# Kernel tuning notes

Measured on AMD Instinct MI355X. Metric: run time of the kernel, lower is better.

The kernel has to match this reference:

```python
import jax, jax.numpy as jnp
import numpy as np

EPS_GIN = 0.0      # GINConv eps (train_eps=False)
EPS_LN = 1e-5      # LayerNorm eps
EPS_GN = 1e-5      # GraphNorm eps


def _layer_norm(h, w, b):
    mu = jnp.mean(h, axis=-1, keepdims=True)
    var = jnp.mean(jnp.square(h - mu), axis=-1, keepdims=True)
    return (h - mu) * jax.lax.rsqrt(var + EPS_LN) * w + b


def setup_inputs() -> dict:
    key = jax.random.key(0)
    ks = jax.random.split(key, 6)
    N, E, C = 50000, 800000, 64
    x = jax.random.normal(ks[0], (N, C), dtype=jnp.float32)
    edge_index = jax.random.randint(ks[1], (2, E), 0, N, dtype=jnp.int64)
    W0 = jax.random.normal(ks[2], (C, C), dtype=jnp.float32) / np.sqrt(C)
    W1 = jax.random.normal(ks[3], (C, C), dtype=jnp.float32) / np.sqrt(C)
    ln0_w = jnp.ones((C,), jnp.float32); ln0_b = jnp.zeros((C,), jnp.float32)
    ln1_w = jnp.ones((C,), jnp.float32); ln1_b = jnp.zeros((C,), jnp.float32)
    # GraphNorm params
    gn_w = jnp.ones((C,), jnp.float32)
    gn_b = jnp.zeros((C,), jnp.float32)
    gn_alpha = jnp.ones((C,), jnp.float32)  # mean_scale
    return {"x": x, "edge_index": edge_index, "W0": W0, "ln0_w": ln0_w,
            "ln0_b": ln0_b, "W1": W1, "ln1_w": ln1_w, "ln1_b": ln1_b,
            "gn_w": gn_w, "gn_b": gn_b, "gn_alpha": gn_alpha}


def reference(x, edge_index, W0, ln0_w, ln0_b, W1, ln1_w, ln1_b, gn_w, gn_b, gn_alpha):
    N = x.shape[0]
    src, dst = edge_index[0], edge_index[1]
    # GINConv aggregation: sum of source-node features at each target node
    agg = jax.ops.segment_sum(x[src], dst, num_segments=N)  # [N, C]
    h = (1.0 + EPS_GIN) * x + agg
    # MLP: (Linear no-bias -> LayerNorm -> ReLU) x 2
    h = jax.nn.relu(_layer_norm(h @ W0.T, ln0_w, ln0_b))
    h = jax.nn.relu(_layer_norm(h @ W1.T, ln1_w, ln1_b))
    # GraphNorm over the single graph (all nodes)
    mean = jnp.mean(h, axis=0, keepdims=True)                # [1, C]
    out = h - gn_alpha * mean
    var = jnp.mean(jnp.square(out), axis=0, keepdims=True)   # [1, C]
    return gn_w * out * jax.lax.rsqrt(var + EPS_GN) + gn_b
```

## Files before the change

kernel.cpp:

```cpp
#include <hip/hip_runtime.h>
#include <hip/hip_fp16.h>
#include <stdint.h>

#define LN_EPS 1e-5f
#define GN_EPS 1e-5f

#define NSB 32
#define SLAB1 36864
#define BE1 2048
#define CH2 18
#define NPB2 32
#define SLAB2 768
#define NFB 2048
#define CAP2 768
#define NSLOT 16

__global__ __launch_bounds__(512) void k_sort1_half(
    const uint32_t* __restrict__ ew, int E, int PB1,
    const float* __restrict__ x, uint4* __restrict__ xh8, int n8,
    int* cursors1, uint32_t* pairs1) {
  __shared__ int whist[8 * NSB];
  __shared__ int wbase[8 * NSB];
  __shared__ int wlcur[8 * NSB];
  __shared__ int binStart[NSB], baseG[NSB];
  __shared__ uint32_t stage[BE1];
  const int t = threadIdx.x;

  if (blockIdx.x >= PB1) {
    int i = (blockIdx.x - PB1) * 512 + t;
    if (i >= n8) return;
    float4 a = *(const float4*)&x[i * 8];
    float4 b = *(const float4*)&x[i * 8 + 4];
    __half2 h0 = __floats2half2_rn(a.x, a.y);
    __half2 h1 = __floats2half2_rn(a.z, a.w);
    __half2 h2 = __floats2half2_rn(b.x, b.y);
    __half2 h3 = __floats2half2_rn(b.z, b.w);
    uint4 o;
    o.x = *(uint32_t*)&h0; o.y = *(uint32_t*)&h1;
    o.z = *(uint32_t*)&h2; o.w = *(uint32_t*)&h3;
    xh8[i] = o;
    return;
  }

  const int w = t >> 6;
  const int e0 = blockIdx.x * BE1;
  const int cnt = min(BE1, E - e0);

  uint32_t v = 0;
  if (t < cnt) v = ew[2 * (e0 + t) + 1];
  const int is32 = __syncthreads_or((int)(v != 0));

  if (t < 8 * NSB) { whist[t] = 0; wlcur[t] = 0; }
  __syncthreads();

  uint32_t myP[4];
  #pragma unroll
  for (int r = 0; r < 4; ++r) {
    int i = t + 512 * r;
    if (i < cnt) {
      long long e = e0 + i;
      int s, d;
      if (is32) {
        s = ((const int*)ew)[e];
        d = ((const int*)ew)[(long long)E + e];
      } else {
        s = (int)((const long long*)ew)[e];
        d = (int)((const long long*)ew)[(long long)E + e];
      }
      myP[r] = ((uint32_t)s << 16) | (uint32_t)d;
      atomicAdd(&whist[w * NSB + (d >> 11)], 1);
    }
  }
  __syncthreads();

  if (t < NSB) {
    int sum = 0;
    #pragma unroll
    for (int w2 = 0; w2 < 8; ++w2) {
      wbase[w2 * NSB + t] = sum;
      sum += whist[w2 * NSB + t];
    }
    int s = sum;
    #pragma unroll
    for (int d = 1; d < NSB; d <<= 1) {
      int o = __shfl_up(s, d, NSB);
      if (t >= d) s += o;
    }
    binStart[t] = s - sum;
    baseG[t] = (sum > 0) ? atomicAdd(&cursors1[t], sum) : 0;
  }
  __syncthreads();

  #pragma unroll
  for (int r = 0; r < 4; ++r) {
    int i = t + 512 * r;
    if (i < cnt) {
      int b = (int)(myP[r] & 0xFFFFu) >> 11;
      int p = binStart[b] + wbase[w * NSB + b] +
              atomicAdd(&wlcur[w * NSB + b], 1);
      stage[p] = myP[r];
    }
  }
  __syncthreads();

  for (int i = t; i < cnt; i += 512) {
    uint32_t pr = stage[i];
    int sb = (int)(pr & 0xFFFFu) >> 11;
    int o = baseG[sb] + (i - binStart[sb]);
    if (o < SLAB1) pairs1[(size_t)sb * SLAB1 + o] = pr;
  }
}

__global__ __launch_bounds__(512) void k_part2(const uint32_t* __restrict__ pairs1,
                                               const int* __restrict__ cursors1,
                                               int* cursors2, uint32_t* pairs2) {
  __shared__ int whist[8 * 64];
  __shared__ int wbase[8 * 64];
  __shared__ int wlcur[8 * 64];
  __shared__ int binStart[64], baseG[64];
  __shared__ uint32_t stage[BE1];
  const int t = threadIdx.x;
  const int w = t >> 6;
  const int sb = blockIdx.x / CH2;
  const int ch = blockIdx.x % CH2;
  const int cntS = min(cursors1[sb], SLAB1);
  const int lo = ch * BE1;
  const int cnt = max(0, min(BE1, cntS - lo));
  const uint32_t* src = pairs1 + (size_t)sb * SLAB1 + lo;

  whist[t] = 0;
  wlcur[t] = 0;
  __syncthreads();

  uint32_t my[4];
  #pragma unroll
  for (int r = 0; r < 4; ++r) {
    int i = t + 512 * r;
    if (i < cnt) {
      my[r] = src[i];
      atomicAdd(&whist[(w << 6) + ((my[r] >> 5) & 63)], 1);
    }
  }
  __syncthreads();

  if (t < 64) {
    int sum = 0;
    #pragma unroll
    for (int w2 = 0; w2 < 8; ++w2) {
      wbase[(w2 << 6) + t] = sum;
      sum += whist[(w2 << 6) + t];
    }
    int s = sum;
    #pragma unroll
    for (int d = 1; d < 64; d <<= 1) {
      int o = __shfl_up(s, d, 64);
      if (t >= d) s += o;
    }
    binStart[t] = s - sum;
    baseG[t] = (sum > 0) ? atomicAdd(&cursors2[(sb << 6) + t], sum) : 0;
  }
  __syncthreads();

  #pragma unroll
  for (int r = 0; r < 4; ++r) {
    int i = t + 512 * r;
    if (i < cnt) {
      int b = (int)(my[r] >> 5) & 63;
      int p = binStart[b] + wbase[(w << 6) + b] +
              atomicAdd(&wlcur[(w << 6) + b], 1);
      stage[p] = my[r];
    }
  }
  __syncthreads();

  for (int i = t; i < cnt; i += 512) {
    uint32_t pr = stage[i];
    int sub = (int)(pr >> 5) & 63;
    int o = baseG[sub] + (i - binStart[sub]);
    if (o < SLAB2) pairs2[(size_t)((sb << 6) + sub) * SLAB2 + o] = pr;
  }
}

__global__ __launch_bounds__(256, 8) void k_fused(
    const float4* __restrict__ x4, const uint4* __restrict__ xh8,
    const uint32_t* __restrict__ pairs, const int* __restrict__ cursors,
    const float* __restrict__ W0g, const float* __restrict__ ln0w,
    const float* __restrict__ ln0b, const float* __restrict__ W1g,
    const float* __restrict__ ln1w, const float* __restrict__ ln1b,
    float* __restrict__ out, int N, float* __restrict__ accum) {
  __shared__ __align__(16) float HYt[64 * 33];
  __shared__ __align__(16) float U[2048];
  int* hist = (int*)U;
  int* offs = hist + 32;
  int* lcur = offs + 32;
  int* list = lcur + 32;
  float* Wt = U;
  float* wsum = U;

  const int t = threadIdx.x;
  const int B = blockIdx.x;
  const int cnt = min(cursors[B], SLAB2);
  const uint32_t* pb = pairs + (size_t)B * SLAB2;
  const int node0 = B * NPB2;

  if (t < 32) hist[t] = 0;
  __syncthreads();

  for (int i = t; i < cnt; i += 256) atomicAdd(&hist[pb[i] & 31], 1);
  __syncthreads();

  if (t < 32) {
    int v = hist[t], s = v;
    #pragma unroll
    for (int d = 1; d < 32; d <<= 1) {
      int o = __shfl_up(s, d, 32);
      if (t >= d) s += o;
    }
    offs[t] = s - v;
    lcur[t] = s - v;
  }
  __syncthreads();

  for (int i = t; i < cnt; i += 256) {
    uint32_t p = pb[i];
    int pos = atomicAdd(&lcur[p & 31], 1);
    if (pos < CAP2) list[pos] = (int)(p >> 16);
  }
  __syncthreads();

  const int q8 = t & 7;
  const int nl = t >> 3;
  const int node = node0 + nl;
  float acc[8] = {};
  if (node < N) {
    float4 sa = x4[node * 16 + 2 * q8];
    float4 sb = x4[node * 16 + 2 * q8 + 1];
    acc[0] = sa.x; acc[1] = sa.y; acc[2] = sa.z; acc[3] = sa.w;
    acc[4] = sb.x; acc[5] = sb.y; acc[6] = sb.z; acc[7] = sb.w;
    int j = offs[nl];
    const int e = min(lcur[nl], CAP2);
    for (; j + 3 < e; j += 4) {
      uint4 v0 = xh8[list[j] * 8 + q8];
      uint4 v1 = xh8[list[j + 1] * 8 + q8];
      uint4 v2 = xh8[list[j + 2] * 8 + q8];
      uint4 v3 = xh8[list[j + 3] * 8 + q8];
      #pragma unroll
      for (int c = 0; c < 4; ++c) {
        uint32_t u0 = (&v0.x)[c], u1 = (&v1.x)[c];
        uint32_t u2 = (&v2.x)[c], u3 = (&v3.x)[c];
        float2 f0 = __half22float2(*(__half2*)&u0);
        float2 f1 = __half22float2(*(__half2*)&u1);
        float2 f2 = __half22float2(*(__half2*)&u2);
        float2 f3 = __half22float2(*(__half2*)&u3);
        acc[2 * c]     += (f0.x + f1.x) + (f2.x + f3.x);
        acc[2 * c + 1] += (f0.y + f1.y) + (f2.y + f3.y);
      }
    }
    for (; j < e; ++j) {
      uint4 v0 = xh8[list[j] * 8 + q8];
      #pragma unroll
      for (int c = 0; c < 4; ++c) {
        uint32_t u0 = (&v0.x)[c];
        float2 f0 = __half22float2(*(__half2*)&u0);
        acc[2 * c] += f0.x;
        acc[2 * c + 1] += f0.y;
      }
    }
  }
  __syncthreads();

  #pragma unroll
  for (int c = 0; c < 8; ++c) HYt[(8 * q8 + c) * 33 + nl] = acc[c];

  const int tx = t & 15;
  const int ty = t >> 4;
  const int wc = t & 63, ww = t >> 6;
  float a0[2][4] = {};

  #pragma unroll
  for (int half = 0; half < 2; ++half) {
    {
      #pragma unroll
      for (int r = 0; r < 2; ++r) {
        int k4 = ww * 4 + 16 * r;
        float4 v = *(const float4*)&W0g[wc * 64 + 32 * half + k4];
        Wt[(k4 + 0) * 64 + wc] = v.x; Wt[(k4 + 1) * 64 + wc] = v.y;
        Wt[(k4 + 2) * 64 + wc] = v.z; Wt[(k4 + 3) * 64 + wc] = v.w;
      }
    }
    __syncthreads();
    #pragma unroll 8
    for (int k = 0; k < 32; ++k) {
      float h0 = HYt[(32 * half + k) * 33 + 2 * ty];
      float h1 = HYt[(32 * half + k) * 33 + 2 * ty + 1];
      float4 wv = *(const float4*)&Wt[k * 64 + 4 * tx];
      a0[0][0] += h0 * wv.x; a0[0][1] += h0 * wv.y;
      a0[0][2] += h0 * wv.z; a0[0][3] += h0 * wv.w;
      a0[1][0] += h1 * wv.x; a0[1][1] += h1 * wv.y;
      a0[1][2] += h1 * wv.z; a0[1][3] += h1 * wv.w;
    }
    __syncthreads();
  }

  {
    const float4 lw = *(const float4*)&ln0w[4 * tx];
    const float4 lb = *(const float4*)&ln0b[4 * tx];
    float y[2][4];
    #pragma unroll
    for (int j = 0; j < 2; ++j) {
      float s = a0[j][0] + a0[j][1] + a0[j][2] + a0[j][3];
      #pragma unroll
      for (int m = 1; m < 16; m <<= 1) s += __shfl_xor(s, m, 16);
      float mu = s * (1.f / 64.f);
      float d0 = a0[j][0] - mu, d1 = a0[j][1] - mu;
      float d2 = a0[j][2] - mu, d3 = a0[j][3] - mu;
      float vv = d0 * d0 + d1 * d1 + d2 * d2 + d3 * d3;
      #pragma unroll
      for (int m = 1; m < 16; m <<= 1) vv += __shfl_xor(vv, m, 16);
      float rs = rsqrtf(vv * (1.f / 64.f) + LN_EPS);
      y[j][0] = fmaxf(d0 * rs * lw.x + lb.x, 0.f);
      y[j][1] = fmaxf(d1 * rs * lw.y + lb.y, 0.f);
      y[j][2] = fmaxf(d2 * rs * lw.z + lb.z, 0.f);
      y[j][3] = fmaxf(d3 * rs * lw.w + lb.w, 0.f);
    }
    #pragma unroll
    for (int j = 0; j < 2; ++j) {
      int n = 2 * ty + j;
      HYt[(4 * tx + 0) * 33 + n] = y[j][0];
      HYt[(4 * tx + 1) * 33 + n] = y[j][1];
      HYt[(4 * tx + 2) * 33 + n] = y[j][2];
      HYt[(4 * tx + 3) * 33 + n] = y[j][3];
    }
  }
  __syncthreads();

  float a1[2][4] = {};
  #pragma unroll
  for (int half = 0; half < 2; ++half) {
    {
      #pragma unroll
      for (int r = 0; r < 2; ++r) {
        int k4 = ww * 4 + 16 * r;
        float4 v = *(const float4*)&W1g[wc * 64 + 32 * half + k4];
        Wt[(k4 + 0) * 64 + wc] = v.x; Wt[(k4 + 1) * 64 + wc] = v.y;
        Wt[(k4 + 2) * 64 + wc] = v.z; Wt[(k4 + 3) * 64 + wc] = v.w;
      }
    }
    __syncthreads();
    #pragma unroll 8
    for (int k = 0; k < 32; ++k) {
      float h0 = HYt[(32 * half + k) * 33 + 2 * ty];
      float h1 = HYt[(32 * half + k) * 33 + 2 * ty + 1];
      float4 wv = *(const float4*)&Wt[k * 64 + 4 * tx];
      a1[0][0] += h0 * wv.x; a1[0][1] += h0 * wv.y;
      a1[0][2] += h0 * wv.z; a1[0][3] += h0 * wv.w;
      a1[1][0] += h1 * wv.x; a1[1][1] += h1 * wv.y;
      a1[1][2] += h1 * wv.z; a1[1][3] += h1 * wv.w;
    }
    __syncthreads();
  }

  const float4 lw = *(const float4*)&ln1w[4 * tx];
  const float4 lb = *(const float4*)&ln1b[4 * tx];
  float st1[4] = {0.f, 0.f, 0.f, 0.f}, st2[4] = {0.f, 0.f, 0.f, 0.f};
  #pragma unroll
  for (int j = 0; j < 2; ++j) {
    int nodej = node0 + 2 * ty + j;
    float s = a1[j][0] + a1[j][1] + a1[j][2] + a1[j][3];
    #pragma unroll
    for (int m = 1; m < 16; m <<= 1) s += __shfl_xor(s, m, 16);
    float mu = s * (1.f / 64.f);
    float d0 = a1[j][0] - mu, d1 = a1[j][1] - mu;
    float d2 = a1[j][2] - mu, d3 = a1[j][3] - mu;
    float vv = d0 * d0 + d1 * d1 + d2 * d2 + d3 * d3;
    #pragma unroll
    for (int m = 1; m < 16; m <<= 1) vv += __shfl_xor(vv, m, 16);
    float rs = rsqrtf(vv * (1.f / 64.f) + LN_EPS);
    float y0 = fmaxf(d0 * rs * lw.x + lb.x, 0.f);
    float y1 = fmaxf(d1 * rs * lw.y + lb.y, 0.f);
    float y2 = fmaxf(d2 * rs * lw.z + lb.z, 0.f);
    float y3 = fmaxf(d3 * rs * lw.w + lb.w, 0.f);
    if (nodej < N) {
      *(float4*)&out[(long long)nodej * 64 + 4 * tx] =
          make_float4(y0, y1, y2, y3);
      st1[0] += y0; st2[0] += y0 * y0;
      st1[1] += y1; st2[1] += y1 * y1;
      st1[2] += y2; st2[2] += y2 * y2;
      st1[3] += y3; st2[3] += y3 * y3;
    }
  }
  #pragma unroll
  for (int i = 0; i < 4; ++i) {
    st1[i] += __shfl_xor(st1[i], 16, 64); st1[i] += __shfl_xor(st1[i], 32, 64);
    st2[i] += __shfl_xor(st2[i], 16, 64); st2[i] += __shfl_xor(st2[i], 32, 64);
  }
  const int lane = t & 63, w = t >> 6;
  if (lane < 16) {
    #pragma unroll
    for (int i = 0; i < 4; ++i) {
      wsum[w * 128 + 4 * lane + i] = st1[i];
      wsum[w * 128 + 64 + 4 * lane + i] = st2[i];
    }
  }
  __syncthreads();
  if (t < 128) {
    float s = wsum[t] + wsum[128 + t] + wsum[256 + t] + wsum[384 + t];
    atomicAdd(&accum[(B & (NSLOT - 1)) * 128 + t], s);
  }
}

__global__ __launch_bounds__(256) void k_apply(
    const float4* __restrict__ h4, const float* __restrict__ accum,
    const float* __restrict__ alpha, const float* __restrict__ gnw,
    const float* __restrict__ gnb, float4* __restrict__ outp, int N) {
  __shared__ float cs[128];
  __shared__ float ab[128];
  const int t = threadIdx.x;
  if (t < 128) {
    float s = 0.f;
    #pragma unroll
    for (int sl = 0; sl < NSLOT; ++sl) s += accum[sl * 128 + t];
    cs[t] = s;
  }
  __syncthreads();
  if (t < 64) {
    float invN = 1.f / (float)N;
    float mu = cs[t] * invN;
    float e2 = cs[64 + t] * invN;
    float al = alpha[t];
    float var = e2 - 2.f * al * mu * mu + al * al * mu * mu;
    float a = gnw[t] * rsqrtf(var + GN_EPS);
    ab[t] = a;
    ab[64 + t] = gnb[t] - a * al * mu;
  }
  __syncthreads();
  int idx = blockIdx.x * 256 + t;
  if (idx < N * 16) {
    int q = idx & 15;
    float4 a = *(const float4*)&ab[q * 4];
    float4 b = *(const float4*)&ab[64 + q * 4];
    float4 h = h4[idx];
    outp[idx] = make_float4(a.x * h.x + b.x, a.y * h.y + b.y, a.z * h.z + b.z,
                            a.w * h.w + b.w);
  }
}

extern "C" void kernel_launch(void* const* d_in, const int* in_sizes, int n_in,
                              void* d_out, int out_size, void* d_ws,
                              size_t ws_size, hipStream_t stream) {
  const float* x    = (const float*)d_in[0];
  const void* edges = d_in[1];
  const float* W0   = (const float*)d_in[2];
  const float* ln0w = (const float*)d_in[3];
  const float* ln0b = (const float*)d_in[4];
  const float* W1   = (const float*)d_in[5];
  const float* ln1w = (const float*)d_in[6];
  const float* ln1b = (const float*)d_in[7];
  const float* gnw  = (const float*)d_in[8];
  const float* gnb  = (const float*)d_in[9];
  const float* gna  = (const float*)d_in[10];
  const int N = in_sizes[0] / 64;
  const int E = in_sizes[1] / 2;
  const int nsbU = (N + 2047) >> 11;
  const int nfbU = nsbU << 6;
  const int PB1 = (E + BE1 - 1) / BE1;
  const int HB  = (N * 8 + 511) / 512;

  float* h         = (float*)d_ws;
  uint32_t* pairs1 = (uint32_t*)d_ws;
  uint32_t* pairs2 = (uint32_t*)(h + (size_t)N * 64);
  uint4* xh8       = (uint4*)(pairs2 + (size_t)NFB * SLAB2);
  int* cursors1    = (int*)(xh8 + (size_t)N * 8);
  int* cursors2    = cursors1 + NSB;
  float* accum     = (float*)(cursors2 + NFB);

  hipMemsetAsync(cursors1, 0, (size_t)(NSB + NFB + NSLOT * 128) * 4, stream);
  k_sort1_half<<<PB1 + HB, 512, 0, stream>>>((const uint32_t*)edges, E, PB1,
                                             x, xh8, N * 8, cursors1, pairs1);
  k_part2<<<nsbU * CH2, 512, 0, stream>>>(pairs1, cursors1, cursors2, pairs2);
  k_fused<<<nfbU, 256, 0, stream>>>((const float4*)x, xh8, pairs2, cursors2,
                                    W0, ln0w, ln0b, W1, ln1w, ln1b, h, N,
                                    accum);
  k_apply<<<(N * 16 + 255) / 256, 256, 0, stream>>>((const float4*)h, accum,
                                                    gna, gnw, gnb,
                                                    (float4*)d_out, N);
}
```

Measured before the change: 142.0 us.

## Replace two-pass global edge partition with per-block buckets scanned in fused kernel

Drops the second partition kernel and the global atomic cursors. Each sort block now writes its edges into fixed-capacity per-(block, 1024-node bin) buckets and records the counts, and each fused block scans all source blocks' buckets for its bin, filtering by sub-bin and building per-node lists in LDS. This removes a kernel launch, a memset and a full pass over the pairs, but each fused block reads 32x more pair data than it keeps. The fixed caps of 88 per bucket and 48 per node can silently drop edges under skew. The HYt pitch also changes to 34 so the matmul loop can read float2 values.

```diff
diff --git a/kernel.cpp b/kernel.cpp
--- a/kernel.cpp
+++ b/kernel.cpp
@@ -5,28 +5,29 @@
 #define LN_EPS 1e-5f
 #define GN_EPS 1e-5f
 
-#define NSB 32
-#define SLAB1 36864
+#define NSB 64
 #define BE1 2048
-#define CH2 18
+#define CAP1R 88
 #define NPB2 32
-#define SLAB2 768
-#define NFB 2048
-#define CAP2 768
+#define CAPN 48
 #define NSLOT 16
 
 __global__ __launch_bounds__(512) void k_sort1_half(
     const uint32_t* __restrict__ ew, int E, int PB1,
     const float* __restrict__ x, uint4* __restrict__ xh8, int n8,
-    int* cursors1, uint32_t* pairs1) {
+    float* __restrict__ accum, int* __restrict__ counts1,
+    uint32_t* __restrict__ pairs1) {
   __shared__ int whist[8 * NSB];
   __shared__ int wbase[8 * NSB];
   __shared__ int wlcur[8 * NSB];
-  __shared__ int binStart[NSB], baseG[NSB];
+  __shared__ int binStart[NSB];
   __shared__ uint32_t stage[BE1];
   const int t = threadIdx.x;
 
   if (blockIdx.x >= PB1) {
+    if (blockIdx.x == PB1) {
+      for (int i = t; i < NSLOT * 128; i += 512) accum[i] = 0.f;
+    }
     int i = (blockIdx.x - PB1) * 512 + t;
     if (i >= n8) return;
     float4 a = *(const float4*)&x[i * 8];
@@ -42,15 +43,17 @@
     return;
   }
 
+  const int b = blockIdx.x;
   const int w = t >> 6;
-  const int e0 = blockIdx.x * BE1;
+  const int e0 = b * BE1;
   const int cnt = min(BE1, E - e0);
 
   uint32_t v = 0;
   if (t < cnt) v = ew[2 * (e0 + t) + 1];
   const int is32 = __syncthreads_or((int)(v != 0));
 
-  if (t < 8 * NSB) { whist[t] = 0; wlcur[t] = 0; }
+  whist[t] = 0;
+  wlcur[t] = 0;
   __syncthreads();
 
   uint32_t myP[4];
@@ -68,7 +71,7 @@
         d = (int)((const long long*)ew)[(long long)E + e];
       }
       myP[r] = ((uint32_t)s << 16) | (uint32_t)d;
-      atomicAdd(&whist[w * NSB + (d >> 11)], 1);
+      atomicAdd(&whist[w * NSB + (d >> 10)], 1);
     }
   }
   __syncthreads();
@@ -83,11 +86,11 @@
     int s = sum;
     #pragma unroll
     for (int d = 1; d < NSB; d <<= 1) {
-      int o = __shfl_up(s, d, NSB);
+      int o = __shfl_up(s, d, 64);
       if (t >= d) s += o;
     }
     binStart[t] = s - sum;
-    baseG[t] = (sum > 0) ? atomicAdd(&cursors1[t], sum) : 0;
+    counts1[t * PB1 + b] = sum;
   }
   __syncthreads();
 
@@ -95,9 +98,9 @@
   for (int r = 0; r < 4; ++r) {
     int i = t + 512 * r;
     if (i < cnt) {
-      int b = (int)(myP[r] & 0xFFFFu) >> 11;
-      int p = binStart[b] + wbase[w * NSB + b] +
-              atomicAdd(&wlcur[w * NSB + b], 1);
+      int b2 = (int)(myP[r] & 0xFFFFu) >> 10;
+      int p = binStart[b2] + wbase[w * NSB + b2] +
+              atomicAdd(&wlcur[w * NSB + b2], 1);
       stage[p] = myP[r];
     }
   }
@@ -105,126 +108,51 @@
 
   for (int i = t; i < cnt; i += 512) {
     uint32_t pr = stage[i];
-    int sb = (int)(pr & 0xFFFFu) >> 11;
-    int o = baseG[sb] + (i - binStart[sb]);
-    if (o < SLAB1) pairs1[(size_t)sb * SLAB1 + o] = pr;
-  }
-}
-
-__global__ __launch_bounds__(512) void k_part2(const uint32_t* __restrict__ pairs1,
-                                               const int* __restrict__ cursors1,
-                                               int* cursors2, uint32_t* pairs2) {
-  __shared__ int whist[8 * 64];
-  __shared__ int wbase[8 * 64];
-  __shared__ int wlcur[8 * 64];
-  __shared__ int binStart[64], baseG[64];
-  __shared__ uint32_t stage[BE1];
-  const int t = threadIdx.x;
-  const int w = t >> 6;
-  const int sb = blockIdx.x / CH2;
-  const int ch = blockIdx.x % CH2;
-  const int cntS = min(cursors1[sb], SLAB1);
-  const int lo = ch * BE1;
-  const int cnt = max(0, min(BE1, cntS - lo));
-  const uint32_t* src = pairs1 + (size_t)sb * SLAB1 + lo;
-
-  whist[t] = 0;
-  wlcur[t] = 0;
-  __syncthreads();
-
-  uint32_t my[4];
-  #pragma unroll
-  for (int r = 0; r < 4; ++r) {
-    int i = t + 512 * r;
-    if (i < cnt) {
-      my[r] = src[i];
-      atomicAdd(&whist[(w << 6) + ((my[r] >> 5) & 63)], 1);
-    }
-  }
-  __syncthreads();
-
-  if (t < 64) {
-    int sum = 0;
-    #pragma unroll
-    for (int w2 = 0; w2 < 8; ++w2) {
-      wbase[(w2 << 6) + t] = sum;
-      sum += whist[(w2 << 6) + t];
-    }
-    int s = sum;
-    #pragma unroll
-    for (int d = 1; d < 64; d <<= 1) {
-      int o = __shfl_up(s, d, 64);
-      if (t >= d) s += o;
-    }
-    binStart[t] = s - sum;
-    baseG[t] = (sum > 0) ? atomicAdd(&cursors2[(sb << 6) + t], sum) : 0;
-  }
-  __syncthreads();
-
-  #pragma unroll
-  for (int r = 0; r < 4; ++r) {
-    int i = t + 512 * r;
-    if (i < cnt) {
-      int b = (int)(my[r] >> 5) & 63;
-      int p = binStart[b] + wbase[(w << 6) + b] +
-              atomicAdd(&wlcur[(w << 6) + b], 1);
-      stage[p] = my[r];
-    }
-  }
-  __syncthreads();
-
-  for (int i = t; i < cnt; i += 512) {
-    uint32_t pr = stage[i];
-    int sub = (int)(pr >> 5) & 63;
-    int o = baseG[sub] + (i - binStart[sub]);
-    if (o < SLAB2) pairs2[(size_t)((sb << 6) + sub) * SLAB2 + o] = pr;
+    int sb = (int)(pr & 0xFFFFu) >> 10;
+    int rel = i - binStart[sb];
+    if (rel < CAP1R) pairs1[((size_t)b * NSB + sb) * CAP1R + rel] = pr;
   }
 }
 
 __global__ __launch_bounds__(256, 8) void k_fused(
     const float4* __restrict__ x4, const uint4* __restrict__ xh8,
-    const uint32_t* __restrict__ pairs, const int* __restrict__ cursors,
-    const float* __restrict__ W0g, const float* __restrict__ ln0w,
+    const uint32_t* __restrict__ pairs1, const int* __restrict__ counts1,
+    int PB1, const float* __restrict__ W0g, const float* __restrict__ ln0w,
     const float* __restrict__ ln0b, const float* __restrict__ W1g,
     const float* __restrict__ ln1w, const float* __restrict__ ln1b,
     float* __restrict__ out, int N, float* __restrict__ accum) {
-  __shared__ __align__(16) float HYt[64 * 33];
+  __shared__ __align__(16) float HYt[64 * 34];
   __shared__ __align__(16) float U[2048];
-  int* hist = (int*)U;
-  int* offs = hist + 32;
-  int* lcur = offs + 32;
-  int* list = lcur + 32;
+  int* list32 = (int*)U;
+  int* cnt32 = (int*)U + 32 * CAPN;
+  int* cLDS = (int*)U + 32 * CAPN + 32;
   float* Wt = U;
   float* wsum = U;
 
   const int t = threadIdx.x;
   const int B = blockIdx.x;
-  const int cnt = min(cursors[B], SLAB2);
-  const uint32_t* pb = pairs + (size_t)B * SLAB2;
+  const int sb = B >> 5;
+  const int sub = B & 31;
   const int node0 = B * NPB2;
 
-  if (t < 32) hist[t] = 0;
-  __syncthreads();
-
-  for (int i = t; i < cnt; i += 256) atomicAdd(&hist[pb[i] & 31], 1);
-  __syncthreads();
-
-  if (t < 32) {
-    int v = hist[t], s = v;
-    #pragma unroll
-    for (int d = 1; d < 32; d <<= 1) {
-      int o = __shfl_up(s, d, 32);
-      if (t >= d) s += o;
-    }
-    offs[t] = s - v;
-    lcur[t] = s - v;
-  }
-  __syncthreads();
-
-  for (int i = t; i < cnt; i += 256) {
-    uint32_t p = pb[i];
-    int pos = atomicAdd(&lcur[p & 31], 1);
-    if (pos < CAP2) list[pos] = (int)(p >> 16);
+  if (t < 32) cnt32[t] = 0;
+  for (int i = t; i < PB1; i += 256) cLDS[i] = counts1[sb * PB1 + i];
+  __syncthreads();
+
+  {
+    const int ln64 = t & 63, w4 = t >> 6;
+    for (int blk = w4; blk < PB1; blk += 4) {
+      int c = cLDS[blk];
+      const uint32_t* rp = pairs1 + ((size_t)blk * NSB + sb) * CAP1R;
+      for (int i = ln64; i < c; i += 64) {
+        uint32_t pr = rp[i];
+        if ((int)((pr >> 5) & 31) == sub) {
+          int nloc = (int)(pr & 31);
+          int pos = atomicAdd(&cnt32[nloc], 1);
+          if (pos < CAPN) list32[nloc * CAPN + pos] = (int)(pr >> 16);
+        }
+      }
+    }
   }
   __syncthreads();
 
@@ -234,16 +162,17 @@
   float acc[8] = {};
   if (node < N) {
     float4 sa = x4[node * 16 + 2 * q8];
-    float4 sb = x4[node * 16 + 2 * q8 + 1];
+    float4 sb2 = x4[node * 16 + 2 * q8 + 1];
     acc[0] = sa.x; acc[1] = sa.y; acc[2] = sa.z; acc[3] = sa.w;
-    acc[4] = sb.x; acc[5] = sb.y; acc[6] = sb.z; acc[7] = sb.w;
-    int j = offs[nl];
-    const int e = min(lcur[nl], CAP2);
+    acc[4] = sb2.x; acc[5] = sb2.y; acc[6] = sb2.z; acc[7] = sb2.w;
+    const int e = min(cnt32[nl], CAPN);
+    const int* lp = list32 + nl * CAPN;
+    int j = 0;
     for (; j + 3 < e; j += 4) {
-      uint4 v0 = xh8[list[j] * 8 + q8];
-      uint4 v1 = xh8[list[j + 1] * 8 + q8];
-      uint4 v2 = xh8[list[j + 2] * 8 + q8];
-      uint4 v3 = xh8[list[j + 3] * 8 + q8];
+      uint4 v0 = xh8[lp[j] * 8 + q8];
+      uint4 v1 = xh8[lp[j + 1] * 8 + q8];
+      uint4 v2 = xh8[lp[j + 2] * 8 + q8];
+      uint4 v3 = xh8[lp[j + 3] * 8 + q8];
       #pragma unroll
       for (int c = 0; c < 4; ++c) {
         uint32_t u0 = (&v0.x)[c], u1 = (&v1.x)[c];
@@ -257,7 +186,7 @@
       }
     }
     for (; j < e; ++j) {
-      uint4 v0 = xh8[list[j] * 8 + q8];
+      uint4 v0 = xh8[lp[j] * 8 + q8];
       #pragma unroll
       for (int c = 0; c < 4; ++c) {
         uint32_t u0 = (&v0.x)[c];
@@ -270,7 +199,7 @@
   __syncthreads();
 
   #pragma unroll
-  for (int c = 0; c < 8; ++c) HYt[(8 * q8 + c) * 33 + nl] = acc[c];
+  for (int c = 0; c < 8; ++c) HYt[(8 * q8 + c) * 34 + nl] = acc[c];
 
   const int tx = t & 15;
   const int ty = t >> 4;
@@ -291,13 +220,12 @@
     __syncthreads();
     #pragma unroll 8
     for (int k = 0; k < 32; ++k) {
-      float h0 = HYt[(32 * half + k) * 33 + 2 * ty];
-      float h1 = HYt[(32 * half + k) * 33 + 2 * ty + 1];
+      float2 hh = *(const float2*)&HYt[(32 * half + k) * 34 + 2 * ty];
       float4 wv = *(const float4*)&Wt[k * 64 + 4 * tx];
-      a0[0][0] += h0 * wv.x; a0[0][1] += h0 * wv.y;
-      a0[0][2] += h0 * wv.z; a0[0][3] += h0 * wv.w;
-      a0[1][0] += h1 * wv.x; a0[1][1] += h1 * wv.y;
-      a0[1][2] += h1 * wv.z; a0[1][3] += h1 * wv.w;
+      a0[0][0] += hh.x * wv.x; a0[0][1] += hh.x * wv.y;
+      a0[0][2] += hh.x * wv.z; a0[0][3] += hh.x * wv.w;
+      a0[1][0] += hh.y * wv.x; a0[1][1] += hh.y * wv.y;
+      a0[1][2] += hh.y * wv.z; a0[1][3] += hh.y * wv.w;
     }
     __syncthreads();
   }
@@ -326,10 +254,10 @@
     #pragma unroll
     for (int j = 0; j < 2; ++j) {
       int n = 2 * ty + j;
-      HYt[(4 * tx + 0) * 33 + n] = y[j][0];
-      HYt[(4 * tx + 1) * 33 + n] = y[j][1];
-      HYt[(4 * tx + 2) * 33 + n] = y[j][2];
-      HYt[(4 * tx + 3) * 33 + n] = y[j][3];
+      HYt[(4 * tx + 0) * 34 + n] = y[j][0];
+      HYt[(4 * tx + 1) * 34 + n] = y[j][1];
+      HYt[(4 * tx + 2) * 34 + n] = y[j][2];
+      HYt[(4 * tx + 3) * 34 + n] = y[j][3];
     }
   }
   __syncthreads();
@@ -349,13 +277,12 @@
     __syncthreads();
     #pragma unroll 8
     for (int k = 0; k < 32; ++k) {
-      float h0 = HYt[(32 * half + k) * 33 + 2 * ty];
-      float h1 = HYt[(32 * half + k) * 33 + 2 * ty + 1];
+      float2 hh = *(const float2*)&HYt[(32 * half + k) * 34 + 2 * ty];
       float4 wv = *(const float4*)&Wt[k * 64 + 4 * tx];
-      a1[0][0] += h0 * wv.x; a1[0][1] += h0 * wv.y;
-      a1[0][2] += h0 * wv.z; a1[0][3] += h0 * wv.w;
-      a1[1][0] += h1 * wv.x; a1[1][1] += h1 * wv.y;
-      a1[1][2] += h1 * wv.z; a1[1][3] += h1 * wv.w;
+      a1[0][0] += hh.x * wv.x; a1[0][1] += hh.x * wv.y;
+      a1[0][2] += hh.x * wv.z; a1[0][3] += hh.x * wv.w;
+      a1[1][0] += hh.y * wv.x; a1[1][1] += hh.y * wv.y;
+      a1[1][2] += hh.y * wv.z; a1[1][3] += hh.y * wv.w;
     }
     __syncthreads();
   }
@@ -461,25 +388,22 @@
   const float* gna  = (const float*)d_in[10];
   const int N = in_sizes[0] / 64;
   const int E = in_sizes[1] / 2;
-  const int nsbU = (N + 2047) >> 11;
-  const int nfbU = nsbU << 6;
   const int PB1 = (E + BE1 - 1) / BE1;
   const int HB  = (N * 8 + 511) / 512;
+  const int nsb = (N + 1023) >> 10;
+  const int nfbU = nsb * 32;
 
   float* h         = (float*)d_ws;
-  uint32_t* pairs1 = (uint32_t*)d_ws;
-  uint32_t* pairs2 = (uint32_t*)(h + (size_t)N * 64);
-  uint4* xh8       = (uint4*)(pairs2 + (size_t)NFB * SLAB2);
-  int* cursors1    = (int*)(xh8 + (size_t)N * 8);
-  int* cursors2    = cursors1 + NSB;
-  float* accum     = (float*)(cursors2 + NFB);
-
-  hipMemsetAsync(cursors1, 0, (size_t)(NSB + NFB + NSLOT * 128) * 4, stream);
+  uint4* xh8       = (uint4*)(h + (size_t)N * 64);
+  uint32_t* pairs1 = (uint32_t*)(xh8 + (size_t)N * 8);
+  int* counts1     = (int*)(pairs1 + (size_t)PB1 * NSB * CAP1R);
+  float* accum     = (float*)(counts1 + (size_t)NSB * PB1);
+
   k_sort1_half<<<PB1 + HB, 512, 0, stream>>>((const uint32_t*)edges, E, PB1,
-                                             x, xh8, N * 8, cursors1, pairs1);
-  k_part2<<<nsbU * CH2, 512, 0, stream>>>(pairs1, cursors1, cursors2, pairs2);
-  k_fused<<<nfbU, 256, 0, stream>>>((const float4*)x, xh8, pairs2, cursors2,
-                                    W0, ln0w, ln0b, W1, ln1w, ln1b, h, N,
+                                             x, xh8, N * 8, accum, counts1,
+                                             pairs1);
+  k_fused<<<nfbU, 256, 0, stream>>>((const float4*)x, xh8, pairs1, counts1,
+                                    PB1, W0, ln0w, ln0b, W1, ln1w, ln1b, h, N,
                                     accum);
   k_apply<<<(N * 16 + 255) / 256, 256, 0, stream>>>((const float4*)h, accum,
                                                     gna, gnw, gnb,
```

After: 167.0 us. 17.6% more time.
